# Kernel tuning notes

Measured on AMD Instinct MI355X. Metric: run time of the kernel, lower is better.

The kernel has to match this reference:

```python
import jax, jax.numpy as jnp
import numpy as np

N_NODES = 100000
N_EDGES = 3200000
N_GRAPHS = 64
IN_DIM = 8
HIDDEN = 128
N_CLASSES = 10


def _glorot(key, fan_in, fan_out):
    s = 1.0 / np.sqrt(fan_in)
    return jax.random.uniform(key, (fan_in, fan_out), jnp.float32, -s, s)


def setup_inputs() -> dict:
    key = jax.random.key(0)
    ks = jax.random.split(key, 16)
    x = jax.random.normal(ks[0], (N_NODES, IN_DIM), jnp.float32)
    edge_index = jax.random.randint(ks[1], (2, N_EDGES), 0, N_NODES, jnp.int64)
    batch = jnp.sort(jax.random.randint(ks[2], (N_NODES,), 0, N_GRAPHS, jnp.int64))
    inp = {"x": x, "edge_index": edge_index, "batch": batch}
    dims = [(IN_DIM, HIDDEN)] + [(HIDDEN, HIDDEN)] * 4
    for i, (fi, fo) in enumerate(dims, start=1):
        inp[f"W{i}"] = _glorot(ks[2 + i], fi, fo)
        inp[f"b{i}"] = jnp.zeros((fo,), jnp.float32)
    inp["Wout"] = _glorot(ks[10], HIDDEN, N_CLASSES)
    inp["bout"] = jnp.zeros((N_CLASSES,), jnp.float32)
    return inp


def reference(x, edge_index, batch, W1, b1, W2, b2, W3, b3, W4, b4, W5, b5, Wout, bout):
    src, dst = edge_index[0], edge_index[1]
    E = src.shape[0]
    # GCN symmetric normalization with self-loops: deg computed on dst (col)
    deg = jax.ops.segment_sum(jnp.ones((E,), x.dtype), dst, num_segments=N_NODES) + 1.0
    dis = jax.lax.rsqrt(deg)                      # deg^{-1/2}, [N]
    enorm = dis[src] * dis[dst]                   # per-edge coeff, [E]
    self_coef = 1.0 / deg                         # self-loop coeff, [N]

    def gcn_conv(h, W, b):
        h = h @ W                                 # [N, F_out]
        msg = h[src] * enorm[:, None]             # gather + scale, [E, F_out]
        agg = jax.ops.segment_sum(msg, dst, num_segments=N_NODES)
        agg = agg + self_coef[:, None] * h        # fused self-loop term
        return agg + b

    h = jax.nn.relu(gcn_conv(x, W1, b1))
    h = jax.nn.relu(gcn_conv(h, W2, b2))
    h = jax.nn.relu(gcn_conv(h, W3, b3))
    h = jax.nn.relu(gcn_conv(h, W4, b4))
    h = jax.nn.relu(gcn_conv(h, W5, b5))

    # global mean pool per graph
    counts = jax.ops.segment_sum(jnp.ones((N_NODES,), h.dtype), batch, num_segments=N_GRAPHS)
    sums = jax.ops.segment_sum(h, batch, num_segments=N_GRAPHS)
    pooled = sums / jnp.maximum(counts, 1.0)[:, None]   # [G, HIDDEN]

    logits = pooled @ Wout + bout
    return jax.nn.log_softmax(logits, axis=1)
```

## Files before the change

kernel.cpp:

```cpp
#include <hip/hip_runtime.h>
#include <hip/hip_fp16.h>

#define N_NODES 100000
#define N_EDGES 3200000
#define N_GRAPHS 64
#define HID 128
#define NBUCK 782
#define NPART 256
#define EPB (N_EDGES / NPART)

typedef _Float16 half8 __attribute__((ext_vector_type(8)));
typedef float floatx4 __attribute__((ext_vector_type(4)));
typedef float floatx2 __attribute__((ext_vector_type(2)));

__device__ inline unsigned char f32_to_fp8(float v) {
    int p = __builtin_amdgcn_cvt_pk_fp8_f32(v, v, 0, false);
    return (unsigned char)(p & 0xff);
}

__global__ __launch_bounds__(256) void hist_kernel(const int* __restrict__ dst,
                                                   int* __restrict__ hist_g) {
    __shared__ int lh[NBUCK];
    int t = threadIdx.x, b = blockIdx.x;
    for (int j = t; j < NBUCK; j += 256) lh[j] = 0;
    __syncthreads();
    int beg = b * EPB, end = beg + EPB;
    for (int i = beg + t; i < end; i += 256) atomicAdd(&lh[dst[i] >> 7], 1);
    __syncthreads();
    for (int j = t; j < NBUCK; j += 256) hist_g[j * NPART + b] = lh[j];
}

__global__ __launch_bounds__(256) void tot_kernel(const int* __restrict__ hist_g,
                                                  int* __restrict__ tot) {
    int wave = blockIdx.x * 4 + (threadIdx.x >> 6);
    if (wave >= NBUCK) return;
    int lane = threadIdx.x & 63;
    const int4* h4 = (const int4*)(hist_g + (size_t)wave * NPART);
    int4 v = h4[lane];
    int s = v.x + v.y + v.z + v.w;
    #pragma unroll
    for (int off = 32; off > 0; off >>= 1) s += __shfl_down(s, off, 64);
    if (lane == 0) tot[wave] = s;
}

__global__ __launch_bounds__(1024) void scan_tot(const int* __restrict__ tot,
                                                 int* __restrict__ bb,
                                                 int* __restrict__ row_ptrN) {
    __shared__ int buf[1024];
    int t = threadIdx.x;
    int v = (t < NBUCK) ? tot[t] : 0;
    buf[t] = v;
    __syncthreads();
    for (int off = 1; off < 1024; off <<= 1) {
        int x = (t >= off) ? buf[t - off] : 0;
        __syncthreads();
        buf[t] += x;
        __syncthreads();
    }
    if (t < NBUCK) bb[t] = buf[t] - v;
    if (t == NBUCK - 1) {
        bb[NBUCK] = buf[t];
        row_ptrN[0] = buf[t];
    }
}

__global__ __launch_bounds__(256) void offs_kernel(int* __restrict__ hist_g,
                                                   const int* __restrict__ bb) {
    int wave = blockIdx.x * 4 + (threadIdx.x >> 6);
    if (wave >= NBUCK) return;
    int lane = threadIdx.x & 63;
    int4* h4 = (int4*)(hist_g + (size_t)wave * NPART);
    int4 v = h4[lane];
    int s = v.x + v.y + v.z + v.w;
    int e = s;
    #pragma unroll
    for (int off = 1; off < 64; off <<= 1) {
        int x = __shfl_up(e, off, 64);
        if (lane >= off) e += x;
    }
    e -= s;
    int base = bb[wave] + e;
    int4 o;
    o.x = base; base += v.x;
    o.y = base; base += v.y;
    o.z = base; base += v.z;
    o.w = base;
    h4[lane] = o;
}

__global__ __launch_bounds__(256) void part_kernel(const int* __restrict__ src,
                                                   const int* __restrict__ dst,
                                                   const int* __restrict__ hist_g,
                                                   int2* __restrict__ ebuf) {
    __shared__ int lf[NBUCK];
    int t = threadIdx.x, b = blockIdx.x;
    for (int j = t; j < NBUCK; j += 256) lf[j] = hist_g[j * NPART + b];
    __syncthreads();
    int beg = b * EPB, end = beg + EPB;
    for (int i = beg + t; i < end; i += 256) {
        int s = src[i], d = dst[i];
        int pos = atomicAdd(&lf[d >> 7], 1);
        ebuf[pos] = make_int2(s, d);
    }
}

__global__ __launch_bounds__(256) void build_kernel(const int2* __restrict__ ebuf,
                                                    const int* __restrict__ bb,
                                                    int* __restrict__ row_ptr,
                                                    int* __restrict__ col,
                                                    float* __restrict__ dis, int n) {
    __shared__ int c[128], fl[128], sc[128];
    int t = threadIdx.x, k = blockIdx.x;
    if (t < 128) c[t] = 0;
    __syncthreads();
    int beg = bb[k], end = bb[k + 1];
    for (int i = beg + t; i < end; i += 256) atomicAdd(&c[ebuf[i].y & 127], 1);
    __syncthreads();
    if (t < 128) sc[t] = c[t];
    __syncthreads();
    for (int off = 1; off < 128; off <<= 1) {
        int x = (t >= off && t < 128) ? sc[t - off] : 0;
        __syncthreads();
        if (t < 128) sc[t] += x;
        __syncthreads();
    }
    if (t < 128) {
        int rb = beg + sc[t] - c[t];
        fl[t] = rb;
        int node = k * 128 + t;
        if (node < n) {
            row_ptr[node] = rb;
            dis[node] = rsqrtf((float)c[t] + 1.0f);
        }
    }
    __syncthreads();
    for (int i = beg + t; i < end; i += 256) {
        int2 e = ebuf[i];
        int pos = atomicAdd(&fl[e.y & 127], 1);
        col[pos] = e.x;
    }
}

__global__ void prep_kernel(const float* __restrict__ x, const float* __restrict__ dis,
                            __half* __restrict__ g1, int n) {
    int i = blockIdx.x * blockDim.x + threadIdx.x;
    if (i < n) {
        float ds = dis[i];
        const float4* xr = (const float4*)(x + (size_t)i * 8);
        float4 x0 = xr[0], x1 = xr[1];
        __half2 h0 = __floats2half2_rn(ds * x0.x, ds * x0.y);
        __half2 h1 = __floats2half2_rn(ds * x0.z, ds * x0.w);
        __half2 h2 = __floats2half2_rn(ds * x1.x, ds * x1.y);
        __half2 h3 = __floats2half2_rn(ds * x1.z, ds * x1.w);
        uint2 v0, v1;
        v0.x = *(unsigned*)&h0; v0.y = *(unsigned*)&h1;
        v1.x = *(unsigned*)&h2; v1.y = *(unsigned*)&h3;
        uint2* o = (uint2*)(g1 + (size_t)i * 8);
        o[0] = v0; o[1] = v1;
    }
}

__global__ __launch_bounds__(256) void agg1_kernel(const __half* __restrict__ g1,
                                                   const int* __restrict__ row_ptr,
                                                   const int* __restrict__ col,
                                                   const float* __restrict__ dis,
                                                   float* __restrict__ p, int n) {
    int node = blockIdx.x * 4 + (threadIdx.x >> 6);
    if (node >= n) return;
    int lane = threadIdx.x & 63;
    int grp = lane >> 2;
    int fid = lane & 3;
    int beg = row_ptr[node], end = row_ptr[node + 1];
    float a0 = 0.f, a1 = 0.f;
    for (int e0 = beg; e0 < end; e0 += 16) {
        int m = end - e0;
        if (grp < m) {
            int c = col[e0 + grp];
            __half2 h2 = *(const __half2*)(g1 + (size_t)c * 8 + fid * 2);
            float2 f = __half22float2(h2);
            a0 += f.x; a1 += f.y;
        }
    }
    a0 += __shfl_xor(a0, 4);  a1 += __shfl_xor(a1, 4);
    a0 += __shfl_xor(a0, 8);  a1 += __shfl_xor(a1, 8);
    a0 += __shfl_xor(a0, 16); a1 += __shfl_xor(a1, 16);
    a0 += __shfl_xor(a0, 32); a1 += __shfl_xor(a1, 32);
    if (lane < 4) {
        __half2 own = *(const __half2*)(g1 + (size_t)node * 8 + fid * 2);
        float2 fo = __half22float2(own);
        float d = dis[node];
        *(float2*)(p + (size_t)node * 8 + fid * 2) = make_float2(d * (a0 + fo.x), d * (a1 + fo.y));
    }
}

__device__ inline uint2 f4_to_h4(float4 v) {
    __half2 a = __floats2half2_rn(v.x, v.y);
    __half2 b = __floats2half2_rn(v.z, v.w);
    uint2 r;
    r.x = *(unsigned*)&a;
    r.y = *(unsigned*)&b;
    return r;
}

__global__ __launch_bounds__(256) void gemm_k8(const float* __restrict__ A,
                                               const float* __restrict__ W,
                                               const float* __restrict__ bias,
                                               __half* __restrict__ out, int n) {
    __shared__ float4 Ws[8 * 32];
    const float4* W4 = (const float4*)W;
    for (int i = threadIdx.x; i < 8 * 32; i += 256) Ws[i] = W4[i];
    __syncthreads();
    int r = blockIdx.x * 256 + threadIdx.x;
    if (r >= n) return;
    float4 acc[32];
    #pragma unroll
    for (int j = 0; j < 32; j++) acc[j] = make_float4(0.f, 0.f, 0.f, 0.f);
    const float4* Arow = (const float4*)(A + (size_t)r * 8);
    float4 a0 = Arow[0], a1 = Arow[1];
    float av[8] = {a0.x, a0.y, a0.z, a0.w, a1.x, a1.y, a1.z, a1.w};
    #pragma unroll
    for (int kk = 0; kk < 8; kk++) {
        float a = av[kk];
        #pragma unroll
        for (int j = 0; j < 32; j++) {
            float4 w = Ws[kk * 32 + j];
            acc[j].x += a * w.x;
            acc[j].y += a * w.y;
            acc[j].z += a * w.z;
            acc[j].w += a * w.w;
        }
    }
    uint2* o = (uint2*)(out + (size_t)r * HID);
    const float4* b4 = (const float4*)bias;
    #pragma unroll
    for (int j = 0; j < 32; j++) {
        float4 b = b4[j];
        float4 v = make_float4(fmaxf(acc[j].x + b.x, 0.f), fmaxf(acc[j].y + b.y, 0.f),
                               fmaxf(acc[j].z + b.z, 0.f), fmaxf(acc[j].w + b.w, 0.f));
        o[j] = f4_to_h4(v);
    }
}

__global__ __launch_bounds__(128) void wconv(const float* __restrict__ W,
                                             __half* __restrict__ Wt) {
    int j = blockIdx.x, k = threadIdx.x;
    Wt[j * 128 + k] = __float2half(W[k * 128 + j]);
}

__global__ __launch_bounds__(256) void gemm_mfma(const __half* __restrict__ A,
                                                 const __half* __restrict__ Wt,
                                                 const float* __restrict__ dis,
                                                 unsigned char* __restrict__ outq, int n) {
    __shared__ uint4 wt_lds[128 * 17];
    __shared__ uint4 a_lds[64 * 17];
    int t = threadIdx.x;
    const uint4* Wg = (const uint4*)Wt;
    #pragma unroll
    for (int i = 0; i < 8; i++) {
        int idx = i * 256 + t;
        int j = idx >> 4, kq = idx & 15;
        wt_lds[j * 17 + kq] = Wg[idx];
    }
    int base = blockIdx.x * 64;
    const uint4* Ag = (const uint4*)A;
    #pragma unroll
    for (int i = 0; i < 4; i++) {
        int idx = i * 256 + t;
        int r = idx >> 4, kq = idx & 15;
        int row = base + r;
        if (row >= n) row = n - 1;
        a_lds[r * 17 + kq] = Ag[(size_t)row * 16 + kq];
    }
    __syncthreads();
    int w = t >> 6, lane = t & 63;
    int m = lane & 15, quad = lane >> 4;
    floatx4 acc[8];
    #pragma unroll
    for (int jt = 0; jt < 8; jt++) acc[jt] = (floatx4)(0.f);
    #pragma unroll
    for (int kc = 0; kc < 4; kc++) {
        uint4 araw = a_lds[(w * 16 + m) * 17 + kc * 4 + quad];
        half8 af = *(half8*)&araw;
        #pragma unroll
        for (int jt = 0; jt < 8; jt++) {
            uint4 braw = wt_lds[(jt * 16 + m) * 17 + kc * 4 + quad];
            half8 bf = *(half8*)&braw;
            acc[jt] = __builtin_amdgcn_mfma_f32_16x16x32_f16(af, bf, acc[jt], 0, 0, 0);
        }
    }
    #pragma unroll
    for (int reg = 0; reg < 4; reg++) {
        int row = base + w * 16 + quad * 4 + reg;
        if (row < n) {
            float ds = dis[row];
            #pragma unroll
            for (int jt = 0; jt < 8; jt++) {
                outq[(size_t)row * 128 + jt * 16 + m] = f32_to_fp8(acc[jt][reg] * ds);
            }
        }
    }
}

__global__ __launch_bounds__(256) void agg_kernel(const unsigned char* __restrict__ gq,
                                                  const int* __restrict__ row_ptr,
                                                  const int* __restrict__ col,
                                                  const float* __restrict__ dis,
                                                  const float* __restrict__ bias,
                                                  __half* __restrict__ out, int n) {
    int node = blockIdx.x * 4 + (threadIdx.x >> 6);
    if (node >= n) return;
    int lane = threadIdx.x & 63;
    int grp = lane >> 4;
    int fl = (lane & 15) * 8;
    int beg = row_ptr[node], end = row_ptr[node + 1];
    floatx2 a01 = {0.f, 0.f}, a23 = {0.f, 0.f}, a45 = {0.f, 0.f}, a67 = {0.f, 0.f};
    for (int e0 = beg; e0 < end; e0 += 64) {
        int m = min(64, end - e0);
        int cl = (lane < m) ? col[e0 + lane] : 0;
        int full = m >> 4;
        for (int j = 0; j < full; j++) {
            int c[4];
            #pragma unroll
            for (int u = 0; u < 4; u++) c[u] = __shfl(cl, j * 16 + u * 4 + grp);
            uint2 raw[4];
            #pragma unroll
            for (int u = 0; u < 4; u++)
                raw[u] = *(const uint2*)(gq + (size_t)c[u] * 128 + fl);
            #pragma unroll
            for (int u = 0; u < 4; u++) {
                a01 += __builtin_amdgcn_cvt_pk_f32_fp8(raw[u].x, false);
                a23 += __builtin_amdgcn_cvt_pk_f32_fp8(raw[u].x, true);
                a45 += __builtin_amdgcn_cvt_pk_f32_fp8(raw[u].y, false);
                a67 += __builtin_amdgcn_cvt_pk_f32_fp8(raw[u].y, true);
            }
        }
        for (int j4 = full * 16; j4 < m; j4 += 4) {
            int idx = j4 + grp;
            int c = __shfl(cl, idx & 63);
            float val = (idx < m) ? 1.f : 0.f;
            uint2 raw = *(const uint2*)(gq + (size_t)c * 128 + fl);
            floatx2 f0 = __builtin_amdgcn_cvt_pk_f32_fp8(raw.x, false);
            floatx2 f1 = __builtin_amdgcn_cvt_pk_f32_fp8(raw.x, true);
            floatx2 f2 = __builtin_amdgcn_cvt_pk_f32_fp8(raw.y, false);
            floatx2 f3 = __builtin_amdgcn_cvt_pk_f32_fp8(raw.y, true);
            a01 += val * f0;
            a23 += val * f1;
            a45 += val * f2;
            a67 += val * f3;
        }
    }
    float a[8] = {a01[0], a01[1], a23[0], a23[1], a45[0], a45[1], a67[0], a67[1]};
    #pragma unroll
    for (int k = 0; k < 8; k++) {
        a[k] += __shfl_xor(a[k], 16);
        a[k] += __shfl_xor(a[k], 32);
    }
    if (lane < 16) {
        float d = dis[node];
        uint2 own = *(const uint2*)(gq + (size_t)node * 128 + fl);
        floatx2 s0 = __builtin_amdgcn_cvt_pk_f32_fp8(own.x, false);
        floatx2 s1 = __builtin_amdgcn_cvt_pk_f32_fp8(own.x, true);
        floatx2 s2 = __builtin_amdgcn_cvt_pk_f32_fp8(own.y, false);
        floatx2 s3 = __builtin_amdgcn_cvt_pk_f32_fp8(own.y, true);
        float sv[8] = {s0[0], s0[1], s1[0], s1[1], s2[0], s2[1], s3[0], s3[1]};
        float4 b0 = *(const float4*)(bias + fl);
        float4 b1 = *(const float4*)(bias + fl + 4);
        float bv[8] = {b0.x, b0.y, b0.z, b0.w, b1.x, b1.y, b1.z, b1.w};
        float o[8];
        #pragma unroll
        for (int k = 0; k < 8; k++) o[k] = fmaxf(d * (a[k] + sv[k]) + bv[k], 0.f);
        uint4 q;
        __half2 q0 = __floats2half2_rn(o[0], o[1]);
        __half2 q1 = __floats2half2_rn(o[2], o[3]);
        __half2 q2 = __floats2half2_rn(o[4], o[5]);
        __half2 q3 = __floats2half2_rn(o[6], o[7]);
        q.x = *(unsigned*)&q0;
        q.y = *(unsigned*)&q1;
        q.z = *(unsigned*)&q2;
        q.w = *(unsigned*)&q3;
        *(uint4*)(out + (size_t)node * HID + fl) = q;
    }
}

__global__ __launch_bounds__(128) void gbounds_kernel(const int* __restrict__ batch,
                                                      int* __restrict__ bnd,
                                                      int* __restrict__ gcnt) {
    int g = threadIdx.x;
    if (g <= N_GRAPHS) {
        int lo = 0, hi = N_NODES;
        while (lo < hi) {
            int mid = (lo + hi) >> 1;
            if (batch[mid] < g) lo = mid + 1;
            else hi = mid;
        }
        bnd[g] = lo;
    }
    __syncthreads();
    if (g < N_GRAPHS) gcnt[g] = bnd[g + 1] - bnd[g];
}

__global__ __launch_bounds__(128) void pool_kernel(const __half* __restrict__ h,
                                                   const int* __restrict__ batch,
                                                   float* __restrict__ pooled, int n) {
    int f = threadIdx.x;
    int n0 = blockIdx.x * 64;
    if (n0 >= n) return;
    int n1 = min(n0 + 64, n);
    float acc = 0.f;
    int cur = batch[n0];
    for (int i = n0; i < n1; i++) {
        int b = batch[i];
        if (b != cur) {
            atomicAdd(&pooled[cur * HID + f], acc);
            acc = 0.f;
            cur = b;
        }
        acc += __half2float(h[(size_t)i * HID + f]);
    }
    atomicAdd(&pooled[cur * HID + f], acc);
}

__global__ __launch_bounds__(128) void final_kernel(const float* __restrict__ pooled,
                                                    const int* __restrict__ gcnt,
                                                    const float* __restrict__ Wout,
                                                    const float* __restrict__ bout,
                                                    float* __restrict__ out) {
    __shared__ float p[HID];
    __shared__ float lg[10];
    __shared__ float lsum;
    int g = blockIdx.x, t = threadIdx.x;
    float c = fmaxf((float)gcnt[g], 1.0f);
    p[t] = pooled[g * HID + t] / c;
    __syncthreads();
    if (t < 10) {
        float s = bout[t];
        for (int f = 0; f < HID; f++) s += p[f] * Wout[f * 10 + t];
        lg[t] = s;
    }
    __syncthreads();
    if (t == 0) {
        float m = lg[0];
        for (int ci = 1; ci < 10; ci++) m = fmaxf(m, lg[ci]);
        float se = 0.f;
        for (int ci = 0; ci < 10; ci++) se += expf(lg[ci] - m);
        lsum = m + logf(se);
    }
    __syncthreads();
    if (t < 10) out[g * 10 + t] = lg[t] - lsum;
}

extern "C" void kernel_launch(void* const* d_in, const int* in_sizes, int n_in,
                              void* d_out, int out_size, void* d_ws, size_t ws_size,
                              hipStream_t stream) {
    const float* x = (const float*)d_in[0];
    const int* ei = (const int*)d_in[1];
    const int* batch = (const int*)d_in[2];
    const float* W[5] = {(const float*)d_in[3], (const float*)d_in[5], (const float*)d_in[7],
                         (const float*)d_in[9], (const float*)d_in[11]};
    const float* B[5] = {(const float*)d_in[4], (const float*)d_in[6], (const float*)d_in[8],
                         (const float*)d_in[10], (const float*)d_in[12]};
    const float* Wout = (const float*)d_in[13];
    const float* bout = (const float*)d_in[14];
    float* out = (float*)d_out;

    const int* src = ei;
    const int* dst = ei + N_EDGES;

    char* ws = (char*)d_ws;
    size_t off = 0;
    auto alloc = [&](size_t bytes) -> char* {
        char* p = ws + off;
        off = (off + bytes + 255) & ~(size_t)255;
        return p;
    };
    float* pooled = (float*)alloc(N_GRAPHS * HID * 4);
    size_t zero_span = off;
    int* gcnt = (int*)alloc(N_GRAPHS * 4);
    int* bnd = (int*)alloc((N_GRAPHS + 1) * 4);
    int* row_ptr = (int*)alloc((N_NODES + 1) * 4);
    float* dis = (float*)alloc(N_NODES * 4);
    int* hist_g = (int*)alloc((size_t)NBUCK * NPART * 4);
    int* tot = (int*)alloc(NBUCK * 4);
    int* bb = (int*)alloc((NBUCK + 1) * 4);
    int2* ebuf = (int2*)alloc((size_t)N_EDGES * 8);
    int* col = (int*)alloc((size_t)N_EDGES * 4);
    __half* wt = (__half*)alloc(4 * 128 * 128 * 2);
    __half* g1 = (__half*)alloc((size_t)N_NODES * 8 * 2);
    float* p1 = (float*)alloc((size_t)N_NODES * 8 * 4);
    __half* h_a = (__half*)alloc((size_t)N_NODES * HID * 2);
    unsigned char* gq = (unsigned char*)alloc((size_t)N_NODES * HID);

    hipMemsetAsync(d_ws, 0, zero_span, stream);

    int nb = (N_NODES + 255) / 256;
    int wb = (NBUCK + 3) / 4;

    hist_kernel<<<NPART, 256, 0, stream>>>(dst, hist_g);
    tot_kernel<<<wb, 256, 0, stream>>>(hist_g, tot);
    scan_tot<<<1, 1024, 0, stream>>>(tot, bb, row_ptr + N_NODES);
    offs_kernel<<<wb, 256, 0, stream>>>(hist_g, bb);
    part_kernel<<<NPART, 256, 0, stream>>>(src, dst, hist_g, ebuf);
    build_kernel<<<NBUCK, 256, 0, stream>>>(ebuf, bb, row_ptr, col, dis, N_NODES);

    prep_kernel<<<nb, 256, 0, stream>>>(x, dis, g1, N_NODES);
    gbounds_kernel<<<1, 128, 0, stream>>>(batch, bnd, gcnt);
    for (int l = 1; l < 5; l++)
        wconv<<<128, 128, 0, stream>>>(W[l], wt + (size_t)(l - 1) * 128 * 128);

    int gb = (N_NODES + 255) / 256;
    int ab = (N_NODES + 3) / 4;
    int mb = (N_NODES + 63) / 64;

    agg1_kernel<<<ab, 256, 0, stream>>>(g1, row_ptr, col, dis, p1, N_NODES);
    gemm_k8<<<gb, 256, 0, stream>>>(p1, W[0], B[0], h_a, N_NODES);
    for (int l = 1; l < 5; l++) {
        gemm_mfma<<<mb, 256, 0, stream>>>(h_a, wt + (size_t)(l - 1) * 128 * 128, dis, gq,
                                          N_NODES);
        agg_kernel<<<ab, 256, 0, stream>>>(gq, row_ptr, col, dis, B[l], h_a, N_NODES);
    }

    pool_kernel<<<(N_NODES + 63) / 64, 128, 0, stream>>>(h_a, batch, pooled, N_NODES);
    final_kernel<<<N_GRAPHS, 128, 0, stream>>>(pooled, gcnt, Wout, bout, out);
}
```

Baseline: 558.4 us.

## Pack edge buffer into 32-bit words and widen fp8 gather loads to 16 bytes

The partition buffer now stores each edge as one int, holding the source in the low 17 bits and the destination's low 7 bits above it, which halves ebuf write and read traffic in CSR construction. The aggregation kernel gives each lane 16 fp8 features through uint4 loads, with 8 lanes per row and 8 edges processed in parallel, instead of 8 features through uint2 loads. It reduces with three shuffle stages instead of two and writes two uint4 outputs per lane. Column index loads use nontemporal hints. The trade-off is more registers per lane in the aggregation loop and a packing scheme that only works while node ids fit in 17 bits.

```diff
diff --git a/kernel.cpp b/kernel.cpp
--- a/kernel.cpp
+++ b/kernel.cpp
@@ -91,7 +91,7 @@
 __global__ __launch_bounds__(256) void part_kernel(const int* __restrict__ src,
                                                    const int* __restrict__ dst,
                                                    const int* __restrict__ hist_g,
-                                                   int2* __restrict__ ebuf) {
+                                                   int* __restrict__ ebuf) {
     __shared__ int lf[NBUCK];
     int t = threadIdx.x, b = blockIdx.x;
     for (int j = t; j < NBUCK; j += 256) lf[j] = hist_g[j * NPART + b];
@@ -100,11 +100,11 @@
     for (int i = beg + t; i < end; i += 256) {
         int s = src[i], d = dst[i];
         int pos = atomicAdd(&lf[d >> 7], 1);
-        ebuf[pos] = make_int2(s, d);
-    }
-}
-
-__global__ __launch_bounds__(256) void build_kernel(const int2* __restrict__ ebuf,
+        ebuf[pos] = s | ((d & 127) << 17);
+    }
+}
+
+__global__ __launch_bounds__(256) void build_kernel(const int* __restrict__ ebuf,
                                                     const int* __restrict__ bb,
                                                     int* __restrict__ row_ptr,
                                                     int* __restrict__ col,
@@ -114,7 +114,7 @@
     if (t < 128) c[t] = 0;
     __syncthreads();
     int beg = bb[k], end = bb[k + 1];
-    for (int i = beg + t; i < end; i += 256) atomicAdd(&c[ebuf[i].y & 127], 1);
+    for (int i = beg + t; i < end; i += 256) atomicAdd(&c[(ebuf[i] >> 17) & 127], 1);
     __syncthreads();
     if (t < 128) sc[t] = c[t];
     __syncthreads();
@@ -135,9 +135,9 @@
     }
     __syncthreads();
     for (int i = beg + t; i < end; i += 256) {
-        int2 e = ebuf[i];
-        int pos = atomicAdd(&fl[e.y & 127], 1);
-        col[pos] = e.x;
+        int e = ebuf[i];
+        int pos = atomicAdd(&fl[(e >> 17) & 127], 1);
+        col[pos] = e & 0x1FFFF;
     }
 }
 
@@ -175,7 +175,7 @@
     for (int e0 = beg; e0 < end; e0 += 16) {
         int m = end - e0;
         if (grp < m) {
-            int c = col[e0 + grp];
+            int c = __builtin_nontemporal_load(&col[e0 + grp]);
             __half2 h2 = *(const __half2*)(g1 + (size_t)c * 8 + fid * 2);
             float2 f = __half22float2(h2);
             a0 += f.x; a1 += f.y;
@@ -310,75 +310,106 @@
     int node = blockIdx.x * 4 + (threadIdx.x >> 6);
     if (node >= n) return;
     int lane = threadIdx.x & 63;
-    int grp = lane >> 4;
-    int fl = (lane & 15) * 8;
+    int es = lane >> 3;
+    int fid = lane & 7;
+    size_t fo = (size_t)fid * 16;
     int beg = row_ptr[node], end = row_ptr[node + 1];
-    floatx2 a01 = {0.f, 0.f}, a23 = {0.f, 0.f}, a45 = {0.f, 0.f}, a67 = {0.f, 0.f};
+    floatx2 a[8];
+    #pragma unroll
+    for (int k = 0; k < 8; k++) a[k] = (floatx2){0.f, 0.f};
     for (int e0 = beg; e0 < end; e0 += 64) {
         int m = min(64, end - e0);
-        int cl = (lane < m) ? col[e0 + lane] : 0;
-        int full = m >> 4;
-        for (int j = 0; j < full; j++) {
+        int cl = (lane < m) ? __builtin_nontemporal_load(&col[e0 + lane]) : 0;
+        int full = m >> 3;
+        int j = 0;
+        for (; j + 4 <= full; j += 4) {
             int c[4];
             #pragma unroll
-            for (int u = 0; u < 4; u++) c[u] = __shfl(cl, j * 16 + u * 4 + grp);
-            uint2 raw[4];
+            for (int u = 0; u < 4; u++) c[u] = __shfl(cl, (j + u) * 8 + es);
+            uint4 raw[4];
             #pragma unroll
             for (int u = 0; u < 4; u++)
-                raw[u] = *(const uint2*)(gq + (size_t)c[u] * 128 + fl);
+                raw[u] = *(const uint4*)(gq + (size_t)c[u] * 128 + fo);
             #pragma unroll
             for (int u = 0; u < 4; u++) {
-                a01 += __builtin_amdgcn_cvt_pk_f32_fp8(raw[u].x, false);
-                a23 += __builtin_amdgcn_cvt_pk_f32_fp8(raw[u].x, true);
-                a45 += __builtin_amdgcn_cvt_pk_f32_fp8(raw[u].y, false);
-                a67 += __builtin_amdgcn_cvt_pk_f32_fp8(raw[u].y, true);
+                unsigned rw[4] = {raw[u].x, raw[u].y, raw[u].z, raw[u].w};
+                #pragma unroll
+                for (int h = 0; h < 4; h++) {
+                    a[h * 2] += __builtin_amdgcn_cvt_pk_f32_fp8(rw[h], false);
+                    a[h * 2 + 1] += __builtin_amdgcn_cvt_pk_f32_fp8(rw[h], true);
+                }
             }
         }
-        for (int j4 = full * 16; j4 < m; j4 += 4) {
-            int idx = j4 + grp;
+        for (; j < full; j++) {
+            int c = __shfl(cl, j * 8 + es);
+            uint4 raw = *(const uint4*)(gq + (size_t)c * 128 + fo);
+            unsigned rw[4] = {raw.x, raw.y, raw.z, raw.w};
+            #pragma unroll
+            for (int h = 0; h < 4; h++) {
+                a[h * 2] += __builtin_amdgcn_cvt_pk_f32_fp8(rw[h], false);
+                a[h * 2 + 1] += __builtin_amdgcn_cvt_pk_f32_fp8(rw[h], true);
+            }
+        }
+        int rem0 = full * 8;
+        if (rem0 < m) {
+            int idx = rem0 + es;
             int c = __shfl(cl, idx & 63);
             float val = (idx < m) ? 1.f : 0.f;
-            uint2 raw = *(const uint2*)(gq + (size_t)c * 128 + fl);
-            floatx2 f0 = __builtin_amdgcn_cvt_pk_f32_fp8(raw.x, false);
-            floatx2 f1 = __builtin_amdgcn_cvt_pk_f32_fp8(raw.x, true);
-            floatx2 f2 = __builtin_amdgcn_cvt_pk_f32_fp8(raw.y, false);
-            floatx2 f3 = __builtin_amdgcn_cvt_pk_f32_fp8(raw.y, true);
-            a01 += val * f0;
-            a23 += val * f1;
-            a45 += val * f2;
-            a67 += val * f3;
-        }
-    }
-    float a[8] = {a01[0], a01[1], a23[0], a23[1], a45[0], a45[1], a67[0], a67[1]};
-    #pragma unroll
-    for (int k = 0; k < 8; k++) {
-        a[k] += __shfl_xor(a[k], 16);
-        a[k] += __shfl_xor(a[k], 32);
-    }
-    if (lane < 16) {
+            uint4 raw = *(const uint4*)(gq + (size_t)c * 128 + fo);
+            unsigned rw[4] = {raw.x, raw.y, raw.z, raw.w};
+            #pragma unroll
+            for (int h = 0; h < 4; h++) {
+                a[h * 2] += val * __builtin_amdgcn_cvt_pk_f32_fp8(rw[h], false);
+                a[h * 2 + 1] += val * __builtin_amdgcn_cvt_pk_f32_fp8(rw[h], true);
+            }
+        }
+    }
+    float av[16];
+    #pragma unroll
+    for (int k = 0; k < 8; k++) { av[2 * k] = a[k][0]; av[2 * k + 1] = a[k][1]; }
+    #pragma unroll
+    for (int k = 0; k < 16; k++) {
+        av[k] += __shfl_xor(av[k], 8);
+        av[k] += __shfl_xor(av[k], 16);
+        av[k] += __shfl_xor(av[k], 32);
+    }
+    if (lane < 8) {
         float d = dis[node];
-        uint2 own = *(const uint2*)(gq + (size_t)node * 128 + fl);
-        floatx2 s0 = __builtin_amdgcn_cvt_pk_f32_fp8(own.x, false);
-        floatx2 s1 = __builtin_amdgcn_cvt_pk_f32_fp8(own.x, true);
-        floatx2 s2 = __builtin_amdgcn_cvt_pk_f32_fp8(own.y, false);
-        floatx2 s3 = __builtin_amdgcn_cvt_pk_f32_fp8(own.y, true);
-        float sv[8] = {s0[0], s0[1], s1[0], s1[1], s2[0], s2[1], s3[0], s3[1]};
-        float4 b0 = *(const float4*)(bias + fl);
-        float4 b1 = *(const float4*)(bias + fl + 4);
-        float bv[8] = {b0.x, b0.y, b0.z, b0.w, b1.x, b1.y, b1.z, b1.w};
-        float o[8];
+        uint4 own = *(const uint4*)(gq + (size_t)node * 128 + fo);
+        unsigned ow[4] = {own.x, own.y, own.z, own.w};
+        float sv[16];
         #pragma unroll
-        for (int k = 0; k < 8; k++) o[k] = fmaxf(d * (a[k] + sv[k]) + bv[k], 0.f);
-        uint4 q;
-        __half2 q0 = __floats2half2_rn(o[0], o[1]);
-        __half2 q1 = __floats2half2_rn(o[2], o[3]);
-        __half2 q2 = __floats2half2_rn(o[4], o[5]);
-        __half2 q3 = __floats2half2_rn(o[6], o[7]);
-        q.x = *(unsigned*)&q0;
-        q.y = *(unsigned*)&q1;
-        q.z = *(unsigned*)&q2;
-        q.w = *(unsigned*)&q3;
-        *(uint4*)(out + (size_t)node * HID + fl) = q;
+        for (int h = 0; h < 4; h++) {
+            floatx2 lo = __builtin_amdgcn_cvt_pk_f32_fp8(ow[h], false);
+            floatx2 hi = __builtin_amdgcn_cvt_pk_f32_fp8(ow[h], true);
+            sv[4 * h] = lo[0]; sv[4 * h + 1] = lo[1];
+            sv[4 * h + 2] = hi[0]; sv[4 * h + 3] = hi[1];
+        }
+        float bv[16];
+        #pragma unroll
+        for (int q4 = 0; q4 < 4; q4++) {
+            float4 b = *(const float4*)(bias + fid * 16 + q4 * 4);
+            bv[4 * q4] = b.x; bv[4 * q4 + 1] = b.y; bv[4 * q4 + 2] = b.z; bv[4 * q4 + 3] = b.w;
+        }
+        float o[16];
+        #pragma unroll
+        for (int k = 0; k < 16; k++) o[k] = fmaxf(d * (av[k] + sv[k]) + bv[k], 0.f);
+        uint4 q0, q1;
+        __half2 p0 = __floats2half2_rn(o[0], o[1]);
+        __half2 p1 = __floats2half2_rn(o[2], o[3]);
+        __half2 p2 = __floats2half2_rn(o[4], o[5]);
+        __half2 p3 = __floats2half2_rn(o[6], o[7]);
+        __half2 p4 = __floats2half2_rn(o[8], o[9]);
+        __half2 p5 = __floats2half2_rn(o[10], o[11]);
+        __half2 p6 = __floats2half2_rn(o[12], o[13]);
+        __half2 p7 = __floats2half2_rn(o[14], o[15]);
+        q0.x = *(unsigned*)&p0; q0.y = *(unsigned*)&p1;
+        q0.z = *(unsigned*)&p2; q0.w = *(unsigned*)&p3;
+        q1.x = *(unsigned*)&p4; q1.y = *(unsigned*)&p5;
+        q1.z = *(unsigned*)&p6; q1.w = *(unsigned*)&p7;
+        uint4* op = (uint4*)(out + (size_t)node * HID + fid * 16);
+        op[0] = q0;
+        op[1] = q1;
     }
 }
 
@@ -482,7 +513,7 @@
     int* hist_g = (int*)alloc((size_t)NBUCK * NPART * 4);
     int* tot = (int*)alloc(NBUCK * 4);
     int* bb = (int*)alloc((NBUCK + 1) * 4);
-    int2* ebuf = (int2*)alloc((size_t)N_EDGES * 8);
+    int* ebuf = (int*)alloc((size_t)N_EDGES * 4);
     int* col = (int*)alloc((size_t)N_EDGES * 4);
     __half* wt = (__half*)alloc(4 * 128 * 128 * 2);
     __half* g1 = (__half*)alloc((size_t)N_NODES * 8 * 2);
```

After: 597.3 us. 7.0% more time.
